# Kernel optimization log

Measured on AMD Instinct MI355X. Metric: run time of the kernel, lower is better.

The kernel has to match this reference:

```python
import jax, jax.numpy as jnp
import numpy as np

B, N, D_IN, D_ATTN, D_OUT = 8, 2048, 2048, 64, 2048

def setup_inputs() -> dict:
    key = jax.random.key(0)
    ks = jax.random.split(key, 5)
    x = jax.random.normal(ks[0], (B, N, D_IN), dtype=jnp.float32)
    s_qkv = 1.0 / np.sqrt(D_IN)   # torch nn.Linear default init bound
    W_qkv = jax.random.uniform(ks[1], (D_IN, 3 * D_ATTN), jnp.float32, -s_qkv, s_qkv)
    b_qkv = jax.random.uniform(ks[2], (3 * D_ATTN,), jnp.float32, -s_qkv, s_qkv)
    s_p = 1.0 / np.sqrt(D_ATTN)
    W_proj = jax.random.uniform(ks[3], (D_ATTN, D_OUT), jnp.float32, -s_p, s_p)
    b_proj = jax.random.uniform(ks[4], (D_OUT,), jnp.float32, -s_p, s_p)
    return {"x": x, "W_qkv": W_qkv, "b_qkv": b_qkv, "W_proj": W_proj, "b_proj": b_proj}

def reference(x, W_qkv, b_qkv, W_proj, b_proj):
    # qkv projection: [B,N,3*D_ATTN]
    qkv = x @ W_qkv + b_qkv
    q, k, v = jnp.split(qkv, 3, axis=-1)  # each [B,N,D_ATTN]
    scale = jax.lax.rsqrt(jnp.float32(D_ATTN))
    w = jnp.einsum('bnd,bmd->bnm', q, k) * scale  # [B,N,N]
    a = jax.nn.softmax(w, axis=-1)
    ctx = jnp.einsum('bnm,bmd->bnd', a, v)        # [B,N,D_ATTN]
    return ctx @ W_proj + b_proj                   # [B,N,D_OUT]
```

## Files before the change

### kernel.cpp

```cpp
#include <hip/hip_runtime.h>

typedef __bf16 bf16x8 __attribute__((ext_vector_type(8)));
typedef unsigned short u16x8 __attribute__((ext_vector_type(8)));
typedef unsigned short u16x4 __attribute__((ext_vector_type(4)));
typedef float  f32x4  __attribute__((ext_vector_type(4)));

#define QSCALE 0.1803368801111204f
#define NHALF 2

__device__ __forceinline__ unsigned short f2bf(float f) {
  unsigned int u = __float_as_uint(f);
  u = u + 0x7fffu + ((u >> 16) & 1u);
  return (unsigned short)(u >> 16);
}

#define GLD16(src, dst)                                                        \
  __builtin_amdgcn_global_load_lds(                                            \
      (const __attribute__((address_space(1))) void*)(src),                    \
      (__attribute__((address_space(3))) void*)(dst), 16, 0, 0)


__global__ __launch_bounds__(256) void k_trw(const float* __restrict__ Wq,
                                             const float* __restrict__ Wp,
                                             unsigned short* __restrict__ wqT,
                                             unsigned short* __restrict__ wpT) {
  __shared__ float tile[64][193];
  const int t = threadIdx.x;
  if (blockIdx.x < 32) {
    const int k0 = blockIdx.x * 64;
#pragma unroll
    for (int i = 0; i < 12; ++i) {
      int u = i * 256 + t;
      int row = u / 48, c4 = u % 48;
      float4 v = *(const float4*)(Wq + (size_t)(k0 + row) * 192 + c4 * 4);
      tile[row][c4 * 4 + 0] = v.x; tile[row][c4 * 4 + 1] = v.y;
      tile[row][c4 * 4 + 2] = v.z; tile[row][c4 * 4 + 3] = v.w;
    }
    __syncthreads();
#pragma unroll
    for (int i = 0; i < 6; ++i) {
      int u = i * 256 + t;
      int c = u >> 3, k8 = (u & 7) * 8;
      u16x8 h;
#pragma unroll
      for (int j = 0; j < 8; ++j) h[j] = f2bf(tile[k8 + j][c]);
      *(u16x8*)(wqT + (size_t)c * 2048 + k0 + k8) = h;
    }
  } else {
    const int n0 = (blockIdx.x - 32) * 64;
#pragma unroll
    for (int i = 0; i < 4; ++i) {
      int u = i * 256 + t;
      int dd = u >> 4, c4 = u & 15;
      float4 v = *(const float4*)(Wp + (size_t)dd * 2048 + n0 + c4 * 4);
      tile[dd][c4 * 4 + 0] = v.x; tile[dd][c4 * 4 + 1] = v.y;
      tile[dd][c4 * 4 + 2] = v.z; tile[dd][c4 * 4 + 3] = v.w;
    }
    __syncthreads();
#pragma unroll
    for (int i = 0; i < 2; ++i) {
      int u = i * 256 + t;
      int n = u >> 3, d8 = (u & 7) * 8;
      u16x8 h;
      h[0] = f2bf(tile[d8 + 0][n]); h[1] = f2bf(tile[d8 + 1][n]);
      h[2] = f2bf(tile[d8 + 2][n]); h[3] = f2bf(tile[d8 + 3][n]);
      h[4] = f2bf(tile[d8 + 4][n]); h[5] = f2bf(tile[d8 + 5][n]);
      h[6] = f2bf(tile[d8 + 6][n]); h[7] = f2bf(tile[d8 + 7][n]);
      *(u16x8*)(wpT + (size_t)(n0 + n) * 64 + d8) = h;
    }
  }
}

__global__ __launch_bounds__(512) void k_qkv(const float* __restrict__ x,
                                             const unsigned short* __restrict__ wqT,
                                             const float* __restrict__ b_qkv,
                                             unsigned short* __restrict__ qb,
                                             unsigned short* __restrict__ kb,
                                             unsigned short* __restrict__ vt) {
  __shared__ __align__(16) char lds[65536];
  const int t = threadIdx.x;
  const int lane = t & 63, w = t >> 6;
  const int l15 = lane & 15, l4 = lane >> 4;
  const int wm = w >> 2, wn = w & 3;
  const int m0 = blockIdx.x * 64;

  const int arow = t >> 3;
  const int akc  = (t & 7) * 8;
  const float* xrow = x + (size_t)(m0 + arow) * 2048 + akc;
  const int aoff = arow * 128 + ((akc * 2) ^ ((arow & 7) << 4));

  f32x4 acc[2][3] = {};
  float4 xa0_0, xa1_0, xa0_1, xa1_1;

  auto issueA_0 = [&](int kt) {
    xa0_0 = *(const float4*)(xrow + kt * 64);
    xa1_0 = *(const float4*)(xrow + kt * 64 + 4);
  };
  auto issueA_1 = [&](int kt) {
    xa0_1 = *(const float4*)(xrow + kt * 64);
    xa1_1 = *(const float4*)(xrow + kt * 64 + 4);
  };
  auto writeA_0 = [&]() {
    u16x8 h;
    h[0] = f2bf(xa0_0.x); h[1] = f2bf(xa0_0.y); h[2] = f2bf(xa0_0.z); h[3] = f2bf(xa0_0.w);
    h[4] = f2bf(xa1_0.x); h[5] = f2bf(xa1_0.y); h[6] = f2bf(xa1_0.z); h[7] = f2bf(xa1_0.w);
    *(u16x8*)(lds + 0 * 8192 + aoff) = h;
  };
  auto writeA_1 = [&]() {
    u16x8 h;
    h[0] = f2bf(xa0_1.x); h[1] = f2bf(xa0_1.y); h[2] = f2bf(xa0_1.z); h[3] = f2bf(xa0_1.w);
    h[4] = f2bf(xa1_1.x); h[5] = f2bf(xa1_1.y); h[6] = f2bf(xa1_1.z); h[7] = f2bf(xa1_1.w);
    *(u16x8*)(lds + 1 * 8192 + aoff) = h;
  };
  auto stageB = [&](int kt, int d) {
    char* bbase = lds + 16384 + d * 24576;
#pragma unroll
    for (int p = 0; p < 3; ++p) {
      int L = p * 8192 + (w << 10) + (lane << 4);
      int row = L >> 7;
      int cb = (L & 127) ^ ((row & 7) << 4);
      GLD16((const char*)wqT + (size_t)row * 4096 + kt * 128 + cb,
            bbase + p * 8192 + (w << 10));
    }
  };
  auto compute = [&](int d) {
    const char* aB = lds + d * 8192;
    const char* bB = lds + 16384 + d * 24576;
    __builtin_amdgcn_s_setprio(1);
#pragma unroll
    for (int kk = 0; kk < 2; ++kk) {
      int cb = kk * 64 + l4 * 16;
      bf16x8 af[2], bfr[3];
#pragma unroll
      for (int m = 0; m < 2; ++m) {
        int r = wm * 32 + m * 16 + l15;
        af[m] = *(const bf16x8*)(aB + r * 128 + (cb ^ ((r & 7) << 4)));
      }
#pragma unroll
      for (int n = 0; n < 3; ++n) {
        int r = wn * 48 + n * 16 + l15;
        bfr[n] = *(const bf16x8*)(bB + r * 128 + (cb ^ ((r & 7) << 4)));
      }
#pragma unroll
      for (int m = 0; m < 2; ++m)
#pragma unroll
        for (int n = 0; n < 3; ++n)
          acc[m][n] = __builtin_amdgcn_mfma_f32_16x16x32_bf16(af[m], bfr[n], acc[m][n], 0, 0, 0);
    }
    __builtin_amdgcn_s_setprio(0);
  };

#define QKV_STEP(n, P, DOI, DOS, W)                                    \
  {                                                                    \
    writeA_##P();                                                      \
    if (DOI) issueA_##P((n) + 2);                                      \
    if (DOS) stageB((n) + 1, (P) ^ 1);                                 \
    asm volatile("s_waitcnt vmcnt(" W ") lgkmcnt(0)" ::: "memory");    \
    __builtin_amdgcn_s_barrier();                                      \
    compute(P);                                                        \
    __builtin_amdgcn_s_barrier();                                      \
  }

  issueA_0(0); issueA_1(1); stageB(0, 0);
  for (int kt = 0; kt < 30; kt += 2) {
    QKV_STEP(kt,     0, true, true, "5");
    QKV_STEP(kt + 1, 1, true, true, "5");
  }
  QKV_STEP(30, 0, false, true,  "5");
  QKV_STEP(31, 1, false, false, "0");
#undef QKV_STEP

#pragma unroll
  for (int m = 0; m < 2; ++m)
#pragma unroll
    for (int n = 0; n < 3; ++n) {
      int c = wn * 48 + n * 16 + l15;
      int j = c >> 6, cc = c & 63;
      float bias = b_qkv[c];
      int grow0 = m0 + wm * 32 + m * 16 + l4 * 4;
      if (j == 0) {
#pragma unroll
        for (int r = 0; r < 4; ++r)
          qb[(size_t)(grow0 + r) * 64 + cc] = f2bf((acc[m][n][r] + bias) * QSCALE);
      } else if (j == 1) {
#pragma unroll
        for (int r = 0; r < 4; ++r)
          kb[(size_t)(grow0 + r) * 64 + cc] = f2bf(acc[m][n][r] + bias);
      } else {
        int bbv = grow0 >> 11, nn0 = grow0 & 2047;
        u16x4 h;
        h[0] = f2bf(acc[m][n][0] + bias); h[1] = f2bf(acc[m][n][1] + bias);
        h[2] = f2bf(acc[m][n][2] + bias); h[3] = f2bf(acc[m][n][3] + bias);
        *(u16x4*)(vt + ((size_t)bbv * 64 + cc) * 2048 + nn0) = h;
      }
    }
}

__global__ __launch_bounds__(256) void k_attn(const unsigned short* __restrict__ qb,
                                              const unsigned short* __restrict__ kb,
                                              const unsigned short* __restrict__ vt,
                                              float* __restrict__ ctxp,
                                              float* __restrict__ mlp) {
  __shared__ __align__(16) char lds[32768];
  const int t = threadIdx.x;
  const int lane = t & 63, w = t >> 6;
  const int l15 = lane & 15, l4 = lane >> 4;
  const int bb = blockIdx.y;
  const int half = blockIdx.z;
  const int q0 = blockIdx.x * 64 + w * 16;
  const int kt0 = half * 16;
  const unsigned short* qrow = qb + ((size_t)bb * 2048 + q0 + l15) * 64;
  bf16x8 aq[2];
  aq[0] = *(const bf16x8*)(qrow + l4 * 8);
  aq[1] = *(const bf16x8*)(qrow + 32 + l4 * 8);
  f32x4 ctx[4] = {};
  float m = -1e30f, lsum = 0.f;
  const char* kBase = (const char*)kb + (size_t)bb * 2048 * 128;
  const char* vBase = (const char*)vt + (size_t)bb * 64 * 4096;
  const int srcA = ((l4 & 1) << 5) | l15;
  const int srcB = srcA + 16;
  const bool hi = (l4 >> 1) & 1;

  auto stage = [&](int kt, int d) {
#pragma unroll
    for (int p = 0; p < 2; ++p) {
      int L = p * 4096 + (w << 10) + (lane << 4);
      int row = L >> 7;
      int cb = (L & 127) ^ ((row & 7) << 4);
      GLD16(kBase + (size_t)(kt * 64 + row) * 128 + cb,
            lds + d * 8192 + p * 4096 + (w << 10));
      GLD16(vBase + (size_t)row * 4096 + kt * 128 + cb,
            lds + 16384 + d * 8192 + p * 4096 + (w << 10));
    }
  };

  stage(kt0, 0);
  int d = 0;
  for (int kt = 0; kt < 16; ++kt) {
    if (kt < 15) {
      stage(kt0 + kt + 1, d ^ 1);
      asm volatile("s_waitcnt vmcnt(4)" ::: "memory");
    } else {
      asm volatile("s_waitcnt vmcnt(0)" ::: "memory");
    }
    __builtin_amdgcn_s_barrier();
    const char* sK = lds + d * 8192;
    const char* sV = lds + 16384 + d * 8192;
    f32x4 s[4] = {};
    __builtin_amdgcn_s_setprio(1);
#pragma unroll
    for (int kk = 0; kk < 2; ++kk) {
      int cb = kk * 64 + l4 * 16;
#pragma unroll
      for (int mf = 0; mf < 4; ++mf) {
        int r = mf * 16 + l15;
        bf16x8 kf = *(const bf16x8*)(sK + r * 128 + (cb ^ ((r & 7) << 4)));
        s[mf] = __builtin_amdgcn_mfma_f32_16x16x32_bf16(kf, aq[kk], s[mf], 0, 0, 0);
      }
    }
    __builtin_amdgcn_s_setprio(0);
    float pm = fmaxf(fmaxf(fmaxf(s[0][0], s[0][1]), fmaxf(s[0][2], s[0][3])),
                     fmaxf(fmaxf(s[1][0], s[1][1]), fmaxf(s[1][2], s[1][3])));
    pm = fmaxf(pm, fmaxf(fmaxf(fmaxf(s[2][0], s[2][1]), fmaxf(s[2][2], s[2][3])),
                         fmaxf(fmaxf(s[3][0], s[3][1]), fmaxf(s[3][2], s[3][3]))));
    pm = fmaxf(pm, __shfl_xor(pm, 16));
    pm = fmaxf(pm, __shfl_xor(pm, 32));
    if (!__all(pm <= m + 11.5f)) {
      float mn = fmaxf(m, pm);
      float al = __builtin_exp2f(m - mn);
      m = mn; lsum *= al;
#pragma unroll
      for (int df = 0; df < 4; ++df)
#pragma unroll
        for (int r = 0; r < 4; ++r) ctx[df][r] *= al;
    }
    float lp = 0.f;
#pragma unroll
    for (int mf = 0; mf < 4; ++mf)
#pragma unroll
      for (int r = 0; r < 4; ++r) {
        float p = __builtin_exp2f(s[mf][r] - m);
        s[mf][r] = p;
        lp += p;
      }
    lsum += lp;
    unsigned int pk[4][2];
#pragma unroll
    for (int mf = 0; mf < 4; ++mf) {
      asm("v_cvt_pk_bf16_f32 %0, %1, %2" : "=v"(pk[mf][0]) : "v"(s[mf][0]), "v"(s[mf][1]));
      asm("v_cvt_pk_bf16_f32 %0, %1, %2" : "=v"(pk[mf][1]) : "v"(s[mf][2]), "v"(s[mf][3]));
    }
#pragma unroll
    for (int kk = 0; kk < 2; ++kk) {
      unsigned int q00 = __shfl((int)pk[2 * kk][0], srcA);
      unsigned int q10 = __shfl((int)pk[2 * kk + 1][0], srcA);
      unsigned int q01 = __shfl((int)pk[2 * kk][1], srcA);
      unsigned int q11 = __shfl((int)pk[2 * kk + 1][1], srcA);
      unsigned int r00 = __shfl((int)pk[2 * kk][0], srcB);
      unsigned int r10 = __shfl((int)pk[2 * kk + 1][0], srcB);
      unsigned int r01 = __shfl((int)pk[2 * kk][1], srcB);
      unsigned int r11 = __shfl((int)pk[2 * kk + 1][1], srcB);
      uint4 uu;
      uu.x = hi ? q10 : q00;
      uu.y = hi ? q11 : q01;
      uu.z = hi ? r10 : r00;
      uu.w = hi ? r11 : r01;
      bf16x8 pfrag = *(bf16x8*)&uu;
      int cb = kk * 64 + l4 * 16;
      __builtin_amdgcn_s_setprio(1);
#pragma unroll
      for (int df = 0; df < 4; ++df) {
        int rv = df * 16 + l15;
        bf16x8 vf = *(const bf16x8*)(sV + rv * 128 + (cb ^ ((rv & 7) << 4)));
        ctx[df] = __builtin_amdgcn_mfma_f32_16x16x32_bf16(vf, pfrag, ctx[df], 0, 0, 0);
      }
      __builtin_amdgcn_s_setprio(0);
    }
    __builtin_amdgcn_s_barrier();
    d ^= 1;
  }
  lsum += __shfl_xor(lsum, 16);
  lsum += __shfl_xor(lsum, 32);
  size_t g = (size_t)bb * 2048 + q0 + l15;
#pragma unroll
  for (int df = 0; df < 4; ++df) {
    f32x4 c = ctx[df];
    *(float4*)(ctxp + ((size_t)half * 16384 + g) * 64 + df * 16 + l4 * 4) =
        *(float4*)&c;
  }
  if (l4 == 0) {
    float2 ml = make_float2(m, lsum);
    *(float2*)(mlp + ((size_t)half * 16384 + g) * 2) = ml;
  }
}

__global__ __launch_bounds__(512) void k_proj(const float* __restrict__ ctxp,
                                              const float* __restrict__ mlp,
                                              const unsigned short* __restrict__ wpT,
                                              const float* __restrict__ b_proj,
                                              float* __restrict__ out) {
  __shared__ __align__(16) char lds[81920];
  const int t = threadIdx.x;
  const int lane = t & 63, w = t >> 6;
  const int l15 = lane & 15, l4 = lane >> 4;
  const int m0 = blockIdx.x * 64;

  GLD16((const char*)b_proj + (size_t)(w << 10) + (lane << 4), lds + 8192 + (w << 10));

  {
    int r_ = t >> 3;
    int d8 = (t & 7) * 8;
    size_t g = (size_t)m0 + r_;
    float2 ml0 = *(const float2*)(mlp + g * 2);
    float2 ml1 = *(const float2*)(mlp + ((size_t)16384 + g) * 2);
    float M = fmaxf(ml0.x, ml1.x);
    float a0 = __builtin_exp2f(ml0.x - M), a1 = __builtin_exp2f(ml1.x - M);
    float inv = 1.0f / (ml0.y * a0 + ml1.y * a1);
    a0 *= inv; a1 *= inv;
    const float4* p0 = (const float4*)(ctxp + g * 64 + d8);
    const float4* p1 = (const float4*)(ctxp + ((size_t)16384 + g) * 64 + d8);
    float4 v0a = p0[0], v0b = p0[1], v1a = p1[0], v1b = p1[1];
    u16x8 o;
    o[0] = f2bf(v0a.x * a0 + v1a.x * a1); o[1] = f2bf(v0a.y * a0 + v1a.y * a1);
    o[2] = f2bf(v0a.z * a0 + v1a.z * a1); o[3] = f2bf(v0a.w * a0 + v1a.w * a1);
    o[4] = f2bf(v0b.x * a0 + v1b.x * a1); o[5] = f2bf(v0b.y * a0 + v1b.y * a1);
    o[6] = f2bf(v0b.z * a0 + v1b.z * a1); o[7] = f2bf(v0b.w * a0 + v1b.w * a1);
    *(u16x8*)(lds + r_ * 128 + ((d8 * 2) ^ ((r_ & 7) << 4))) = o;
  }

  auto stageB = [&](int c, int d) {
    char* bbase = lds + 16384 + d * 32768;
#pragma unroll
    for (int p = 0; p < 4; ++p) {
      int L = p * 8192 + t * 16;
      int row = L >> 7;
      int cb = (L & 127) ^ ((row & 7) << 4);
      GLD16((const char*)wpT + (size_t)(c * 256 + row) * 128 + cb,
            bbase + p * 8192 + (w << 10));
    }
  };

  stageB(0, 0); stageB(1, 1);
#pragma unroll
  for (int c = 0; c < 8; ++c) {
    if (c == 0)      asm volatile("s_waitcnt vmcnt(4) lgkmcnt(0)" ::: "memory");
    else if (c == 7) asm volatile("s_waitcnt vmcnt(8) lgkmcnt(0)" ::: "memory");
    else             asm volatile("s_waitcnt vmcnt(12) lgkmcnt(0)" ::: "memory");
    __builtin_amdgcn_s_barrier();
    const char* bB = lds + 16384 + (c & 1) * 32768;
    f32x4 acc[4][2] = {};
    __builtin_amdgcn_s_setprio(1);
#pragma unroll
    for (int kk = 0; kk < 2; ++kk) {
      int cb = kk * 64 + l4 * 16;
      bf16x8 af[4], bfr[2];
#pragma unroll
      for (int m = 0; m < 4; ++m) {
        int r = m * 16 + l15;
        af[m] = *(const bf16x8*)(lds + r * 128 + (cb ^ ((r & 7) << 4)));
      }
#pragma unroll
      for (int n = 0; n < 2; ++n) {
        int r = w * 32 + n * 16 + l15;
        bfr[n] = *(const bf16x8*)(bB + r * 128 + (cb ^ ((r & 7) << 4)));
      }
#pragma unroll
      for (int m = 0; m < 4; ++m)
#pragma unroll
        for (int n = 0; n < 2; ++n)
          acc[m][n] = __builtin_amdgcn_mfma_f32_16x16x32_bf16(bfr[n], af[m], acc[m][n], 0, 0, 0);
    }
    __builtin_amdgcn_s_setprio(0);
#pragma unroll
    for (int m = 0; m < 4; ++m)
#pragma unroll
      for (int n = 0; n < 2; ++n) {
        int grow = m0 + m * 16 + l15;
        int gcol = c * 256 + w * 32 + n * 16 + l4 * 4;
        float4 bias = *(const float4*)(lds + 8192 + gcol * 4);
        float4 o;
        o.x = acc[m][n][0] + bias.x; o.y = acc[m][n][1] + bias.y;
        o.z = acc[m][n][2] + bias.z; o.w = acc[m][n][3] + bias.w;
        *(float4*)(out + (size_t)grow * 2048 + gcol) = o;
      }
    __builtin_amdgcn_s_barrier();
    if (c < 6) stageB(c + 2, c & 1);
  }
}

extern "C" void kernel_launch(void* const* d_in, const int* in_sizes, int n_in,
                              void* d_out, int out_size, void* d_ws, size_t ws_size,
                              hipStream_t stream) {
  const float* x      = (const float*)d_in[0];
  const float* W_qkv  = (const float*)d_in[1];
  const float* b_qkv  = (const float*)d_in[2];
  const float* W_proj = (const float*)d_in[3];
  const float* b_proj = (const float*)d_in[4];
  float* out = (float*)d_out;

  unsigned short* ws   = (unsigned short*)d_ws;
  unsigned short* wqT  = ws;
  unsigned short* wpT  = wqT + (size_t)192 * 2048;
  unsigned short* qb   = wpT + (size_t)2048 * 64;
  unsigned short* kb   = qb  + (size_t)16384 * 64;
  unsigned short* vt   = kb  + (size_t)16384 * 64;
  float* ctxp = (float*)(vt + (size_t)16384 * 64);
  float* mlp  = ctxp + (size_t)NHALF * 16384 * 64;

  k_trw<<<64, 256, 0, stream>>>(W_qkv, W_proj, wqT, wpT);
  k_qkv<<<256, 512, 0, stream>>>(x, wqT, b_qkv, qb, kb, vt);
  k_attn<<<dim3(32, 8, NHALF), 256, 0, stream>>>(qb, kb, vt, ctxp, mlp);
  k_proj<<<256, 512, 0, stream>>>(ctxp, mlp, wpT, b_proj, out);
}
```

Measured before the change: 105.6 us.

## Fuse split-KV attention and output projection into one kernel

Merges the attention kernel and the projection kernel. Each 512-thread block now runs both KV halves as two wave groups, merges their partial softmax state and context through LDS, and then does the output projection directly. This removes the fp32 partial-context round trip through global memory and one kernel launch. In exchange, attention now runs on 256 larger blocks instead of 512, and the larger LDS footprint (about 104 KB) may lower occupancy.

```diff
diff --git a/kernel.cpp b/kernel.cpp
--- a/kernel.cpp
+++ b/kernel.cpp
@@ -6,7 +6,6 @@
 typedef float  f32x4  __attribute__((ext_vector_type(4)));
 
 #define QSCALE 0.1803368801111204f
-#define NHALF 2
 
 __device__ __forceinline__ unsigned short f2bf(float f) {
   unsigned int u = __float_as_uint(f);
@@ -196,19 +195,26 @@
     }
 }
 
-__global__ __launch_bounds__(256) void k_attn(const unsigned short* __restrict__ qb,
-                                              const unsigned short* __restrict__ kb,
-                                              const unsigned short* __restrict__ vt,
-                                              float* __restrict__ ctxp,
-                                              float* __restrict__ mlp) {
-  __shared__ __align__(16) char lds[32768];
+#define P_CTX1 0
+#define P_ML1  16384
+#define P_SA   24576
+#define P_BIAS 32768
+#define P_WPT  40960
+__global__ __launch_bounds__(512) void k_attnproj(const unsigned short* __restrict__ qb,
+                                                  const unsigned short* __restrict__ kb,
+                                                  const unsigned short* __restrict__ vt,
+                                                  const unsigned short* __restrict__ wpT,
+                                                  const float* __restrict__ b_proj,
+                                                  float* __restrict__ out) {
+  __shared__ __align__(16) char lds[106496];
   const int t = threadIdx.x;
   const int lane = t & 63, w = t >> 6;
   const int l15 = lane & 15, l4 = lane >> 4;
+  const int wq = w & 3, wh = w >> 2;
   const int bb = blockIdx.y;
-  const int half = blockIdx.z;
-  const int q0 = blockIdx.x * 64 + w * 16;
-  const int kt0 = half * 16;
+  const int qbase = blockIdx.x * 64;
+  const int q0 = qbase + wq * 16;
+  const int kt0 = wh * 16;
   const unsigned short* qrow = qb + ((size_t)bb * 2048 + q0 + l15) * 64;
   bf16x8 aq[2];
   aq[0] = *(const bf16x8*)(qrow + l4 * 8);
@@ -224,13 +230,13 @@
   auto stage = [&](int kt, int d) {
 #pragma unroll
     for (int p = 0; p < 2; ++p) {
-      int L = p * 4096 + (w << 10) + (lane << 4);
+      int L = p * 4096 + (wq << 10) + (lane << 4);
       int row = L >> 7;
       int cb = (L & 127) ^ ((row & 7) << 4);
       GLD16(kBase + (size_t)(kt * 64 + row) * 128 + cb,
-            lds + d * 8192 + p * 4096 + (w << 10));
+            lds + wh * 32768 + d * 8192 + p * 4096 + (wq << 10));
       GLD16(vBase + (size_t)row * 4096 + kt * 128 + cb,
-            lds + 16384 + d * 8192 + p * 4096 + (w << 10));
+            lds + wh * 32768 + 16384 + d * 8192 + p * 4096 + (wq << 10));
     }
   };
 
@@ -244,8 +250,8 @@
       asm volatile("s_waitcnt vmcnt(0)" ::: "memory");
     }
     __builtin_amdgcn_s_barrier();
-    const char* sK = lds + d * 8192;
-    const char* sV = lds + 16384 + d * 8192;
+    const char* sK = lds + wh * 32768 + d * 8192;
+    const char* sV = lds + wh * 32768 + 16384 + d * 8192;
     f32x4 s[4] = {};
     __builtin_amdgcn_s_setprio(1);
 #pragma unroll
@@ -321,55 +327,9 @@
   }
   lsum += __shfl_xor(lsum, 16);
   lsum += __shfl_xor(lsum, 32);
-  size_t g = (size_t)bb * 2048 + q0 + l15;
-#pragma unroll
-  for (int df = 0; df < 4; ++df) {
-    f32x4 c = ctx[df];
-    *(float4*)(ctxp + ((size_t)half * 16384 + g) * 64 + df * 16 + l4 * 4) =
-        *(float4*)&c;
-  }
-  if (l4 == 0) {
-    float2 ml = make_float2(m, lsum);
-    *(float2*)(mlp + ((size_t)half * 16384 + g) * 2) = ml;
-  }
-}
-
-__global__ __launch_bounds__(512) void k_proj(const float* __restrict__ ctxp,
-                                              const float* __restrict__ mlp,
-                                              const unsigned short* __restrict__ wpT,
-                                              const float* __restrict__ b_proj,
-                                              float* __restrict__ out) {
-  __shared__ __align__(16) char lds[81920];
-  const int t = threadIdx.x;
-  const int lane = t & 63, w = t >> 6;
-  const int l15 = lane & 15, l4 = lane >> 4;
-  const int m0 = blockIdx.x * 64;
-
-  GLD16((const char*)b_proj + (size_t)(w << 10) + (lane << 4), lds + 8192 + (w << 10));
-
-  {
-    int r_ = t >> 3;
-    int d8 = (t & 7) * 8;
-    size_t g = (size_t)m0 + r_;
-    float2 ml0 = *(const float2*)(mlp + g * 2);
-    float2 ml1 = *(const float2*)(mlp + ((size_t)16384 + g) * 2);
-    float M = fmaxf(ml0.x, ml1.x);
-    float a0 = __builtin_exp2f(ml0.x - M), a1 = __builtin_exp2f(ml1.x - M);
-    float inv = 1.0f / (ml0.y * a0 + ml1.y * a1);
-    a0 *= inv; a1 *= inv;
-    const float4* p0 = (const float4*)(ctxp + g * 64 + d8);
-    const float4* p1 = (const float4*)(ctxp + ((size_t)16384 + g) * 64 + d8);
-    float4 v0a = p0[0], v0b = p0[1], v1a = p1[0], v1b = p1[1];
-    u16x8 o;
-    o[0] = f2bf(v0a.x * a0 + v1a.x * a1); o[1] = f2bf(v0a.y * a0 + v1a.y * a1);
-    o[2] = f2bf(v0a.z * a0 + v1a.z * a1); o[3] = f2bf(v0a.w * a0 + v1a.w * a1);
-    o[4] = f2bf(v0b.x * a0 + v1b.x * a1); o[5] = f2bf(v0b.y * a0 + v1b.y * a1);
-    o[6] = f2bf(v0b.z * a0 + v1b.z * a1); o[7] = f2bf(v0b.w * a0 + v1b.w * a1);
-    *(u16x8*)(lds + r_ * 128 + ((d8 * 2) ^ ((r_ & 7) << 4))) = o;
-  }
-
-  auto stageB = [&](int c, int d) {
-    char* bbase = lds + 16384 + d * 32768;
+
+  auto stageB = [&](int c, int dd) {
+    char* bbase = lds + P_WPT + dd * 32768;
 #pragma unroll
     for (int p = 0; p < 4; ++p) {
       int L = p * 8192 + t * 16;
@@ -379,15 +339,54 @@
             bbase + p * 8192 + (w << 10));
     }
   };
-
+  GLD16((const char*)b_proj + (w << 10) + (lane << 4), lds + P_BIAS + (w << 10));
   stageB(0, 0); stageB(1, 1);
+
+  if (wh == 1) {
+    char* cbase = lds + P_CTX1 + (wq << 12);
+#pragma unroll
+    for (int df = 0; df < 4; ++df) {
+      int byte = l15 * 256 + df * 64 + l4 * 16;
+      *(f32x4*)(cbase + (byte ^ ((l15 & 7) << 4))) = ctx[df];
+    }
+    if (l4 == 0)
+      *(float2*)(lds + P_ML1 + wq * 128 + l15 * 8) = make_float2(m, lsum);
+  }
+  asm volatile("s_waitcnt lgkmcnt(0)" ::: "memory");
+  __builtin_amdgcn_sched_barrier(0);
+  __builtin_amdgcn_s_barrier();
+  if (wh == 0) {
+    char* cbase = lds + P_CTX1 + (wq << 12);
+    float2 ml1 = *(const float2*)(lds + P_ML1 + wq * 128 + l15 * 8);
+    float M = fmaxf(m, ml1.x);
+    float a0 = __builtin_exp2f(m - M), a1 = __builtin_exp2f(ml1.x - M);
+    float inv = 1.0f / (lsum * a0 + ml1.y * a1);
+    a0 *= inv; a1 *= inv;
+    int rq = wq * 16 + l15;
+#pragma unroll
+    for (int df = 0; df < 4; ++df) {
+      int byte = l15 * 256 + df * 64 + l4 * 16;
+      f32x4 c1 = *(const f32x4*)(cbase + (byte ^ ((l15 & 7) << 4)));
+      u16x4 h;
+      h[0] = f2bf(ctx[df][0] * a0 + c1[0] * a1);
+      h[1] = f2bf(ctx[df][1] * a0 + c1[1] * a1);
+      h[2] = f2bf(ctx[df][2] * a0 + c1[2] * a1);
+      h[3] = f2bf(ctx[df][3] * a0 + c1[3] * a1);
+      int sbyte = rq * 128 + ((df * 32 + l4 * 8) ^ ((rq & 7) << 4));
+      *(u16x4*)(lds + P_SA + sbyte) = h;
+    }
+  }
+  asm volatile("s_waitcnt lgkmcnt(0)" ::: "memory");
+  __builtin_amdgcn_sched_barrier(0);
+  __builtin_amdgcn_s_barrier();
+
 #pragma unroll
   for (int c = 0; c < 8; ++c) {
     if (c == 0)      asm volatile("s_waitcnt vmcnt(4) lgkmcnt(0)" ::: "memory");
     else if (c == 7) asm volatile("s_waitcnt vmcnt(8) lgkmcnt(0)" ::: "memory");
     else             asm volatile("s_waitcnt vmcnt(12) lgkmcnt(0)" ::: "memory");
     __builtin_amdgcn_s_barrier();
-    const char* bB = lds + 16384 + (c & 1) * 32768;
+    const char* bB = lds + P_WPT + (c & 1) * 32768;
     f32x4 acc[4][2] = {};
     __builtin_amdgcn_s_setprio(1);
 #pragma unroll
@@ -395,9 +394,9 @@
       int cb = kk * 64 + l4 * 16;
       bf16x8 af[4], bfr[2];
 #pragma unroll
-      for (int m = 0; m < 4; ++m) {
-        int r = m * 16 + l15;
-        af[m] = *(const bf16x8*)(lds + r * 128 + (cb ^ ((r & 7) << 4)));
+      for (int mm = 0; mm < 4; ++mm) {
+        int r = mm * 16 + l15;
+        af[mm] = *(const bf16x8*)(lds + P_SA + r * 128 + (cb ^ ((r & 7) << 4)));
       }
 #pragma unroll
       for (int n = 0; n < 2; ++n) {
@@ -405,23 +404,23 @@
         bfr[n] = *(const bf16x8*)(bB + r * 128 + (cb ^ ((r & 7) << 4)));
       }
 #pragma unroll
-      for (int m = 0; m < 4; ++m)
+      for (int mm = 0; mm < 4; ++mm)
 #pragma unroll
         for (int n = 0; n < 2; ++n)
-          acc[m][n] = __builtin_amdgcn_mfma_f32_16x16x32_bf16(bfr[n], af[m], acc[m][n], 0, 0, 0);
+          acc[mm][n] = __builtin_amdgcn_mfma_f32_16x16x32_bf16(bfr[n], af[mm], acc[mm][n], 0, 0, 0);
     }
     __builtin_amdgcn_s_setprio(0);
 #pragma unroll
-    for (int m = 0; m < 4; ++m)
+    for (int mm = 0; mm < 4; ++mm)
 #pragma unroll
       for (int n = 0; n < 2; ++n) {
-        int grow = m0 + m * 16 + l15;
+        int grow = qbase + mm * 16 + l15;
         int gcol = c * 256 + w * 32 + n * 16 + l4 * 4;
-        float4 bias = *(const float4*)(lds + 8192 + gcol * 4);
+        float4 bias = *(const float4*)(lds + P_BIAS + gcol * 4);
         float4 o;
-        o.x = acc[m][n][0] + bias.x; o.y = acc[m][n][1] + bias.y;
-        o.z = acc[m][n][2] + bias.z; o.w = acc[m][n][3] + bias.w;
-        *(float4*)(out + (size_t)grow * 2048 + gcol) = o;
+        o.x = acc[mm][n][0] + bias.x; o.y = acc[mm][n][1] + bias.y;
+        o.z = acc[mm][n][2] + bias.z; o.w = acc[mm][n][3] + bias.w;
+        *(float4*)(out + ((size_t)bb * 2048 + grow) * 2048 + gcol) = o;
       }
     __builtin_amdgcn_s_barrier();
     if (c < 6) stageB(c + 2, c & 1);
@@ -444,11 +443,8 @@
   unsigned short* qb   = wpT + (size_t)2048 * 64;
   unsigned short* kb   = qb  + (size_t)16384 * 64;
   unsigned short* vt   = kb  + (size_t)16384 * 64;
-  float* ctxp = (float*)(vt + (size_t)16384 * 64);
-  float* mlp  = ctxp + (size_t)NHALF * 16384 * 64;
 
   k_trw<<<64, 256, 0, stream>>>(W_qkv, W_proj, wqT, wpT);
   k_qkv<<<256, 512, 0, stream>>>(x, wqT, b_qkv, qb, kb, vt);
-  k_attn<<<dim3(32, 8, NHALF), 256, 0, stream>>>(qb, kb, vt, ctxp, mlp);
-  k_proj<<<256, 512, 0, stream>>>(ctxp, mlp, wpT, b_proj, out);
+  k_attnproj<<<dim3(32, 8), 512, 0, stream>>>(qb, kb, vt, wpT, b_proj, out);
 }
```

Result: faster. 97.18 us (-8.0%).
